# Optimization experiments

Hardware: AMD Instinct MI355X
Metric: run time of the kernel (lower is better)

## Reference

```python
import jax, jax.numpy as jnp
import numpy as np

TREE_DEPTH = 8
N_INTERNAL = 2 ** TREE_DEPTH - 1   # 255
N_LEAVES = 2 ** TREE_DEPTH         # 256
N_CLASSES = 100
N_TREES = 16
BATCH = 8192
D_FEAT = 1024
TEMPERATURE = 1.0


def setup_inputs() -> dict:
    key = jax.random.key(0)
    k1, k2, k3, k4, k5 = jax.random.split(key, 5)
    x = jax.random.normal(k1, (BATCH, D_FEAT), dtype=jnp.float32)
    # scale weights ~1/sqrt(D) so split logits are O(1) (avoids sigmoid saturation)
    split_weights = jax.random.normal(k2, (N_TREES, N_INTERNAL, D_FEAT), dtype=jnp.float32) / np.sqrt(D_FEAT)
    split_bias = jax.random.normal(k3, (N_TREES, N_INTERNAL), dtype=jnp.float32)
    leaf_logits = jax.random.normal(k4, (N_TREES, N_LEAVES, N_CLASSES), dtype=jnp.float32)
    tree_weights = jax.random.normal(k5, (N_TREES,), dtype=jnp.float32)
    return {"x": x, "split_weights": split_weights, "split_bias": split_bias,
            "leaf_logits": leaf_logits, "tree_weights": tree_weights}


def reference(x, split_weights, split_bias, leaf_logits, tree_weights):
    # All internal-node split logits in one contraction: [T, B, N_INTERNAL]
    logits = jnp.einsum('bd,tnd->tbn', x, split_weights) + split_bias[:, None, :]
    split_prob = jax.nn.sigmoid(logits / TEMPERATURE)  # P(go right) per heap node
    T, B = split_prob.shape[0], split_prob.shape[1]
    # Level-order path products. Heap layout: level d occupies nodes [2^d-1, 2^(d+1)-2].
    # Child j of a node splits into (left=2j, right=2j+1) at next level -> interleave.
    mu = jnp.ones((T, B, 1), dtype=x.dtype)
    for d in range(TREE_DEPTH):
        start = 2 ** d - 1
        p = split_prob[:, :, start:start + 2 ** d]          # [T, B, 2^d]
        mu = jnp.stack([mu * (1.0 - p), mu * p], axis=-1)   # left, right
        mu = mu.reshape(T, B, 2 ** (d + 1))
    # mu: [T, B, N_LEAVES] leaf reach probabilities, ordering matches leaf_idx
    leaf_dist = jax.nn.softmax(leaf_logits, axis=-1)        # [T, L, C]
    per_tree = jnp.einsum('tbl,tlc->tbc', mu, leaf_dist)    # [T, B, C]
    w = jax.nn.softmax(tree_weights, axis=0)[:, None, None]
    return (per_tree * w).sum(axis=0)                       # [B, C]
```

## Files before the change

kernel.cpp:

```cpp
#include <hip/hip_runtime.h>
#include <hip/hip_fp16.h>

typedef _Float16 f16;
typedef _Float16 f16x4 __attribute__((ext_vector_type(4)));
typedef _Float16 f16x8 __attribute__((ext_vector_type(8)));
typedef float    f32x4 __attribute__((ext_vector_type(4)));

constexpr int TREES = 16;
constexpr int NNODE = 255;
constexpr int NCLS  = 100;
constexpr int NCPAD = 112;
constexpr int NB    = 8192;
constexpr int DF    = 1024;
constexpr int KTOT  = TREES * 256;

constexpr size_t XH_OFF = 0;
constexpr size_t WH_OFF = XH_OFF + (size_t)NB * DF;
constexpr size_t SD_OFF = WH_OFF + (size_t)TREES * 256 * DF;
constexpr size_t BP_OFF = SD_OFF + (size_t)NCPAD * KTOT;
constexpr size_t PT_OFF_F = (BP_OFF + 8192) / 2;

#define WAIT_VMCNT(n) asm volatile("s_waitcnt vmcnt(" #n ")" ::: "memory")
__device__ __forceinline__ void BAR() {
  asm volatile("" ::: "memory");
  __builtin_amdgcn_s_barrier();
  asm volatile("" ::: "memory");
}

__device__ __forceinline__ void gload_lds16(const f16* g, f16* l) {
  __builtin_amdgcn_global_load_lds(
      (const __attribute__((address_space(1))) void*)g,
      (__attribute__((address_space(3))) void*)l, 16, 0, 0);
}

__global__ void cvt_all_k(const float* __restrict__ x, const float* __restrict__ w,
                          f16* __restrict__ xh, f16* __restrict__ wh) {
  int bid = blockIdx.x;
  if (bid < 4096) {
    int i = bid * 256 + threadIdx.x;
    const float4* s = (const float4*)x + (size_t)i * 2;
    float4 u = s[0], v = s[1];
    f16x8 h = {(f16)u.x, (f16)u.y, (f16)u.z, (f16)u.w,
               (f16)v.x, (f16)v.y, (f16)v.z, (f16)v.w};
    *((f16x8*)xh + i) = h;
  } else {
    int i = (bid - 4096) * 256 + threadIdx.x;
    int flat = i * 8;
    int t = flat >> 18;
    int r = (flat >> 10) & 255;
    int k = flat & 1023;
    f16x8 h;
    if (r < NNODE) {
      const float4* s = (const float4*)(w + ((size_t)(t * NNODE + r) * DF + k));
      float4 u = s[0], v = s[1];
      h = (f16x8){(f16)u.x, (f16)u.y, (f16)u.z, (f16)u.w,
                  (f16)v.x, (f16)v.y, (f16)v.z, (f16)v.w};
    } else {
      h = (f16x8){(f16)0.f, (f16)0.f, (f16)0.f, (f16)0.f,
                  (f16)0.f, (f16)0.f, (f16)0.f, (f16)0.f};
    }
    *((f16x8*)wh + i) = h;
  }
}

__global__ void prep_sdist_k(const float* __restrict__ ll,
                             const float* __restrict__ twin,
                             const float* __restrict__ sb,
                             f16* __restrict__ sdt,
                             float* __restrict__ bp) {
  int wv   = threadIdx.x >> 6;
  int lane = threadIdx.x & 63;
  int id   = blockIdx.x * 4 + wv;
  int t    = id >> 8;
  int node = id & 255;

  float wm = -1e30f;
#pragma unroll
  for (int i = 0; i < 16; ++i) wm = fmaxf(wm, twin[i]);
  float wsum = 0.f;
#pragma unroll
  for (int i = 0; i < 16; ++i) wsum += __expf(twin[i] - wm);
  float wt = __expf(twin[t] - wm) / wsum;

  const float* rowp = ll + (size_t)id * NCLS;
  float v1 = rowp[lane];
  bool has2 = (lane + 64) < NCLS;
  float v2 = has2 ? rowp[lane + 64] : -1e30f;
  float mx = fmaxf(v1, v2);
#pragma unroll
  for (int m = 32; m; m >>= 1) mx = fmaxf(mx, __shfl_xor(mx, m, 64));
  float e1 = __expf(v1 - mx);
  float e2 = has2 ? __expf(v2 - mx) : 0.f;
  float ss = e1 + e2;
#pragma unroll
  for (int m = 32; m; m >>= 1) ss += __shfl_xor(ss, m, 64);
  float inv = wt / ss;

  sdt[(size_t)lane * KTOT + id] = (f16)(e1 * inv);
  if (lane + 64 < NCPAD)
    sdt[(size_t)(lane + 64) * KTOT + id] = has2 ? (f16)(e2 * inv) : (f16)0.f;
  if (lane == 0) bp[id] = (node < NNODE) ? sb[(size_t)t * NNODE + node] : 0.f;
}

__global__ __launch_bounds__(512, 2) void tree_gemm1(
    const f16* __restrict__ xh, const f16* __restrict__ wh,
    const float* __restrict__ biasp, const f16* __restrict__ sdt,
    float* __restrict__ ptree) {
  __shared__ f16 smem[81920];
  char* smb = (char*)smem;

  const int tid  = threadIdx.x;
  const int lane = tid & 63;
  const int wid  = tid >> 6;
  const int l15  = lane & 15;
  const int lq   = lane >> 4;
  const int wrow = (wid >> 2) * 128;
  const int wcol = (wid & 3) * 64;

  int bid  = blockIdx.x;
  int xcd  = bid & 7;
  int idx  = bid >> 3;
  int t    = (xcd & 1) * 8 + (idx & 7);
  int brow = (xcd >> 1) * 8 + (idx >> 3);

  const f16* xsrc = xh + (size_t)brow * 256 * DF;
  const f16* wsrc = wh + (size_t)t * 256 * DF;

  auto stage_half = [&](int kt, int c, int half) {
    f16* Ab = smem + c * 32768;
    f16* Bb = Ab + 16384;
    const f16* xk = xsrc + kt * 64;
    const f16* wk = wsrc + kt * 64;
#pragma unroll
    for (int i = half * 2; i < half * 2 + 2; ++i) {
      int q = i * 512 + tid;
      int r = q >> 3;
      int ci = (q & 7) ^ (r & 7);
      gload_lds16(xk + (size_t)r * DF + ci * 8, Ab + q * 8);
    }
#pragma unroll
    for (int i = half * 2; i < half * 2 + 2; ++i) {
      int q = i * 512 + tid;
      int r = q >> 3;
      int ci = (q & 7) ^ (r & 7);
      gload_lds16(wk + (size_t)r * DF + ci * 8, Bb + q * 8);
    }
  };

  f32x4 acc[8][4];
#pragma unroll
  for (int m = 0; m < 8; ++m)
#pragma unroll
    for (int n = 0; n < 4; ++n) acc[m][n] = (f32x4){0.f, 0.f, 0.f, 0.f};

  stage_half(0, 0, 0);
  stage_half(0, 0, 1);

  for (int kt = 0; kt < 16; ++kt) {
    const int c = kt & 1;
    if (kt < 15) {
      stage_half(kt + 1, c ^ 1, 0);
      WAIT_VMCNT(4);
    } else {
      WAIT_VMCNT(0);
    }
    BAR();

    const char* Ab = smb + c * 65536;
    const char* Bb = Ab + 32768;
#pragma unroll
    for (int s = 0; s < 2; ++s) {
      f16x8 af[8], bf[4];
#pragma unroll
      for (int m = 0; m < 8; ++m) {
        int r = wrow + m * 16 + l15;
        af[m] = *(const f16x8*)(Ab + ((r * 128 + s * 64 + lq * 16) ^ ((r & 7) << 4)));
      }
#pragma unroll
      for (int n = 0; n < 4; ++n) {
        int node = wcol + n * 16 + l15;
        bf[n] = *(const f16x8*)(Bb + ((node * 128 + s * 64 + lq * 16) ^ ((node & 7) << 4)));
      }
      if (s == 0 && kt < 15) stage_half(kt + 1, c ^ 1, 1);
#pragma unroll
      for (int m = 0; m < 8; ++m)
#pragma unroll
        for (int n = 0; n < 4; ++n)
          acc[m][n] = __builtin_amdgcn_mfma_f32_16x16x32_f16(bf[n], af[m], acc[m][n], 0, 0, 0);
    }
    BAR();
  }

  f16x4 ph[8][4];
#pragma unroll
  for (int m = 0; m < 8; ++m) {
#pragma unroll
    for (int n = 0; n < 4; ++n) {
      int col = wcol + n * 16 + lq * 4;
      float4 b4 = *(const float4*)(biasp + t * 256 + col);
#pragma unroll
      for (int reg = 0; reg < 4; ++reg) {
        float bv = (reg == 0) ? b4.x : (reg == 1) ? b4.y : (reg == 2) ? b4.z : b4.w;
        float z = acc[m][n][reg] + bv;
        ph[m][n][reg] = (f16)__builtin_amdgcn_rcpf(1.f + __expf(-z));
      }
    }
  }

  char* Sb = smb;
  char* Ub = smb + 32768;
  char* Pb = smb + 98304;

  auto stage_sdt = [&](int c0, int nrows) {
    int nch = nrows * 32;
    for (int q = tid; q < nch; q += 512) {
      int rr = q >> 5;
      int jj = q & 31;
      gload_lds16(sdt + (size_t)(c0 + rr) * KTOT + t * 256 + ((jj * 8) ^ ((rr & 7) << 3)),
                  smem + q * 8);
    }
  };

  for (int h = 0; h < 2; ++h) {
    if ((wid >> 2) == h) {
#pragma unroll
      for (int m = 0; m < 8; ++m) {
#pragma unroll
        for (int n = 0; n < 4; ++n) {
          int r = m * 16 + l15;
          int colb = (wcol + n * 16 + lq * 4) * 2;
          *(f16x4*)(Pb + ((r * 512 + colb) ^ ((r & 15) << 3))) = ph[m][n];
        }
      }
    }
    __syncthreads();

    {
      int r = tid >> 2;
      int chunk = tid & 3;
      auto PR = [&](int node) -> float {
        return (float)*(const f16*)(Pb + ((r * 512 + node * 2) ^ ((r & 15) << 3)));
      };
      float p0 = PR(0);
      float p1 = PR(1 + (chunk >> 1));
      float pr = ((chunk >> 1) ? p0 : 1.f - p0) * ((chunk & 1) ? p1 : 1.f - p1);
      float p2 = PR(3 + chunk);
      float cur[64];
      {
        float mp = pr * p2;
        cur[1] = mp;
        cur[0] = pr - mp;
      }
#pragma unroll
      for (int d = 3; d <= 7; ++d) {
        int sfan = 1 << (d - 2);
        int nb = (1 << d) - 1 + (chunk << (d - 2));
#pragma unroll
        for (int i = sfan - 1; i >= 0; --i) {
          float p = PR(nb + i);
          float mv = cur[i];
          float mp = mv * p;
          cur[2 * i + 1] = mp;
          cur[2 * i] = mv - mp;
        }
      }
#pragma unroll
      for (int g = 0; g < 8; ++g) {
        f16x8 v;
#pragma unroll
        for (int jj = 0; jj < 8; ++jj) v[jj] = (f16)cur[g * 8 + jj];
        *(f16x8*)(Ub + ((r * 512 + chunk * 128 + g * 16) ^ ((r & 7) << 4))) = v;
      }
    }
    __syncthreads();

    f32x4 acc2[7];
#pragma unroll
    for (int n = 0; n < 7; ++n) acc2[n] = (f32x4){0.f, 0.f, 0.f, 0.f};
    int arow = wid * 16 + l15;

    stage_sdt(0, 64);
    WAIT_VMCNT(0);
    __syncthreads();
#pragma unroll
    for (int n = 0; n < 4; ++n) {
#pragma unroll
      for (int s = 0; s < 8; ++s) {
        f16x8 a = *(const f16x8*)(Ub + ((arow * 512 + s * 64 + lq * 16) ^ ((arow & 7) << 4)));
        int br = n * 16 + l15;
        f16x8 b = *(const f16x8*)(Sb + ((br * 512 + s * 64 + lq * 16) ^ ((br & 7) << 4)));
        acc2[n] = __builtin_amdgcn_mfma_f32_16x16x32_f16(a, b, acc2[n], 0, 0, 0);
      }
    }
    __syncthreads();
    stage_sdt(64, 48);
    WAIT_VMCNT(0);
    __syncthreads();
#pragma unroll
    for (int n = 4; n < 7; ++n) {
#pragma unroll
      for (int s = 0; s < 8; ++s) {
        f16x8 a = *(const f16x8*)(Ub + ((arow * 512 + s * 64 + lq * 16) ^ ((arow & 7) << 4)));
        int br = (n - 4) * 16 + l15;
        f16x8 b = *(const f16x8*)(Sb + ((br * 512 + s * 64 + lq * 16) ^ ((br & 7) << 4)));
        acc2[n] = __builtin_amdgcn_mfma_f32_16x16x32_f16(a, b, acc2[n], 0, 0, 0);
      }
    }

    float* pt = ptree + ((size_t)t * NB + brow * 256 + h * 128) * NCLS;
#pragma unroll
    for (int n = 0; n < 7; ++n) {
      int col = n * 16 + l15;
      if (col < NCLS) {
#pragma unroll
        for (int reg = 0; reg < 4; ++reg) {
          int r = wid * 16 + lq * 4 + reg;
          pt[(size_t)r * NCLS + col] = acc2[n][reg];
        }
      }
    }
    if (h == 0) __syncthreads();
  }
}

__global__ void reduce_k(const float* __restrict__ pt, float* __restrict__ out) {
  int i = blockIdx.x * 256 + threadIdx.x;
  constexpr size_t STRIDE4 = (size_t)NB * NCLS / 4;
  const float4* p = (const float4*)pt + i;
  float4 s = p[0];
#pragma unroll
  for (int t = 1; t < TREES; ++t) {
    float4 v = p[t * STRIDE4];
    s.x += v.x; s.y += v.y; s.z += v.z; s.w += v.w;
  }
  ((float4*)out)[i] = s;
}

extern "C" void kernel_launch(void* const* d_in, const int* in_sizes, int n_in,
                              void* d_out, int out_size, void* d_ws, size_t ws_size,
                              hipStream_t stream) {
  const float* x  = (const float*)d_in[0];
  const float* sw = (const float*)d_in[1];
  const float* sb = (const float*)d_in[2];
  const float* ll = (const float*)d_in[3];
  const float* tw = (const float*)d_in[4];
  float* out = (float*)d_out;

  f16* ws  = (f16*)d_ws;
  f16* xh  = ws + XH_OFF;
  f16* wh  = ws + WH_OFF;
  f16* sdt = ws + SD_OFF;
  float* biasp = (float*)(ws + BP_OFF);
  float* ptree = (float*)d_ws + PT_OFF_F;

  cvt_all_k<<<6144, 256, 0, stream>>>(x, sw, xh, wh);
  prep_sdist_k<<<1024, 256, 0, stream>>>(ll, tw, sb, sdt, biasp);
  tree_gemm1<<<512, 512, 0, stream>>>(xh, wh, biasp, sdt, ptree);
  reduce_k<<<(NB * NCLS / 4) / 256, 256, 0, stream>>>(ptree, out);
}
```

Baseline: 224.8 us.

## Triple-buffer GEMM K-loop, merge prep kernels, prefetch leaf table, vectorize path products

Merges the two preprocessing kernels into one launch. The main GEMM loop moves from a double-buffered 64-wide K step to a triple-buffered 32-wide K step with split loads, explicit lgkmcnt waits, sched barriers and setprio around the MFMA groups. The first leaf-distribution tile is now staged early so its load overlaps the sigmoid and path-product work. The path-product LDS reads are also vectorised with a new swizzle. This adds more barriers per K step and relies on fragile waitcnt counting in exchange for better overlap of loads with compute.

```diff
diff --git a/kernel.cpp b/kernel.cpp
--- a/kernel.cpp
+++ b/kernel.cpp
@@ -21,6 +21,7 @@
 constexpr size_t PT_OFF_F = (BP_OFF + 8192) / 2;
 
 #define WAIT_VMCNT(n) asm volatile("s_waitcnt vmcnt(" #n ")" ::: "memory")
+#define WAIT_LGKM0()  asm volatile("s_waitcnt lgkmcnt(0)" ::: "memory")
 __device__ __forceinline__ void BAR() {
   asm volatile("" ::: "memory");
   __builtin_amdgcn_s_barrier();
@@ -33,8 +34,11 @@
       (__attribute__((address_space(3))) void*)l, 16, 0, 0);
 }
 
-__global__ void cvt_all_k(const float* __restrict__ x, const float* __restrict__ w,
-                          f16* __restrict__ xh, f16* __restrict__ wh) {
+__global__ void prep_all_k(const float* __restrict__ x, const float* __restrict__ w,
+                           const float* __restrict__ ll, const float* __restrict__ twin,
+                           const float* __restrict__ sb,
+                           f16* __restrict__ xh, f16* __restrict__ wh,
+                           f16* __restrict__ sdt, float* __restrict__ bp) {
   int bid = blockIdx.x;
   if (bid < 4096) {
     int i = bid * 256 + threadIdx.x;
@@ -43,7 +47,7 @@
     f16x8 h = {(f16)u.x, (f16)u.y, (f16)u.z, (f16)u.w,
                (f16)v.x, (f16)v.y, (f16)v.z, (f16)v.w};
     *((f16x8*)xh + i) = h;
-  } else {
+  } else if (bid < 6144) {
     int i = (bid - 4096) * 256 + threadIdx.x;
     int flat = i * 8;
     int t = flat >> 18;
@@ -60,46 +64,40 @@
                   (f16)0.f, (f16)0.f, (f16)0.f, (f16)0.f};
     }
     *((f16x8*)wh + i) = h;
+  } else {
+    int wv   = threadIdx.x >> 6;
+    int lane = threadIdx.x & 63;
+    int id   = (bid - 6144) * 4 + wv;
+    int t    = id >> 8;
+    int node = id & 255;
+
+    float wm = -1e30f;
+#pragma unroll
+    for (int i = 0; i < 16; ++i) wm = fmaxf(wm, twin[i]);
+    float wsum = 0.f;
+#pragma unroll
+    for (int i = 0; i < 16; ++i) wsum += __expf(twin[i] - wm);
+    float wt = __expf(twin[t] - wm) / wsum;
+
+    const float* rowp = ll + (size_t)id * NCLS;
+    float v1 = rowp[lane];
+    bool has2 = (lane + 64) < NCLS;
+    float v2 = has2 ? rowp[lane + 64] : -1e30f;
+    float mx = fmaxf(v1, v2);
+#pragma unroll
+    for (int m = 32; m; m >>= 1) mx = fmaxf(mx, __shfl_xor(mx, m, 64));
+    float e1 = __expf(v1 - mx);
+    float e2 = has2 ? __expf(v2 - mx) : 0.f;
+    float ss = e1 + e2;
+#pragma unroll
+    for (int m = 32; m; m >>= 1) ss += __shfl_xor(ss, m, 64);
+    float inv = wt / ss;
+
+    sdt[(size_t)lane * KTOT + id] = (f16)(e1 * inv);
+    if (lane + 64 < NCPAD)
+      sdt[(size_t)(lane + 64) * KTOT + id] = has2 ? (f16)(e2 * inv) : (f16)0.f;
+    if (lane == 0) bp[id] = (node < NNODE) ? sb[(size_t)t * NNODE + node] : 0.f;
   }
-}
-
-__global__ void prep_sdist_k(const float* __restrict__ ll,
-                             const float* __restrict__ twin,
-                             const float* __restrict__ sb,
-                             f16* __restrict__ sdt,
-                             float* __restrict__ bp) {
-  int wv   = threadIdx.x >> 6;
-  int lane = threadIdx.x & 63;
-  int id   = blockIdx.x * 4 + wv;
-  int t    = id >> 8;
-  int node = id & 255;
-
-  float wm = -1e30f;
-#pragma unroll
-  for (int i = 0; i < 16; ++i) wm = fmaxf(wm, twin[i]);
-  float wsum = 0.f;
-#pragma unroll
-  for (int i = 0; i < 16; ++i) wsum += __expf(twin[i] - wm);
-  float wt = __expf(twin[t] - wm) / wsum;
-
-  const float* rowp = ll + (size_t)id * NCLS;
-  float v1 = rowp[lane];
-  bool has2 = (lane + 64) < NCLS;
-  float v2 = has2 ? rowp[lane + 64] : -1e30f;
-  float mx = fmaxf(v1, v2);
-#pragma unroll
-  for (int m = 32; m; m >>= 1) mx = fmaxf(mx, __shfl_xor(mx, m, 64));
-  float e1 = __expf(v1 - mx);
-  float e2 = has2 ? __expf(v2 - mx) : 0.f;
-  float ss = e1 + e2;
-#pragma unroll
-  for (int m = 32; m; m >>= 1) ss += __shfl_xor(ss, m, 64);
-  float inv = wt / ss;
-
-  sdt[(size_t)lane * KTOT + id] = (f16)(e1 * inv);
-  if (lane + 64 < NCPAD)
-    sdt[(size_t)(lane + 64) * KTOT + id] = has2 ? (f16)(e2 * inv) : (f16)0.f;
-  if (lane == 0) bp[id] = (node < NNODE) ? sb[(size_t)t * NNODE + node] : 0.f;
 }
 
 __global__ __launch_bounds__(512, 2) void tree_gemm1(
@@ -126,24 +124,15 @@
   const f16* xsrc = xh + (size_t)brow * 256 * DF;
   const f16* wsrc = wh + (size_t)t * 256 * DF;
 
-  auto stage_half = [&](int kt, int c, int half) {
-    f16* Ab = smem + c * 32768;
-    f16* Bb = Ab + 16384;
-    const f16* xk = xsrc + kt * 64;
-    const f16* wk = wsrc + kt * 64;
-#pragma unroll
-    for (int i = half * 2; i < half * 2 + 2; ++i) {
-      int q = i * 512 + tid;
-      int r = q >> 3;
-      int ci = (q & 7) ^ (r & 7);
-      gload_lds16(xk + (size_t)r * DF + ci * 8, Ab + q * 8);
-    }
-#pragma unroll
-    for (int i = half * 2; i < half * 2 + 2; ++i) {
-      int q = i * 512 + tid;
-      int r = q >> 3;
-      int ci = (q & 7) ^ (r & 7);
-      gload_lds16(wk + (size_t)r * DF + ci * 8, Bb + q * 8);
+  auto stage2 = [&](int kt, int b, int pair) {
+    f16* base = smem + b * 16384 + pair * 8192;
+    const f16* src = (pair == 0 ? xsrc : wsrc) + kt * 32;
+#pragma unroll
+    for (int ch = 0; ch < 2; ++ch) {
+      int u = ch * 512 + tid;
+      int r = u >> 2;
+      int ci = (u & 3) ^ (r & 3);
+      gload_lds16(src + (size_t)r * DF + ci * 8, base + u * 8);
     }
   };
 
@@ -153,58 +142,60 @@
 #pragma unroll
     for (int n = 0; n < 4; ++n) acc[m][n] = (f32x4){0.f, 0.f, 0.f, 0.f};
 
-  stage_half(0, 0, 0);
-  stage_half(0, 0, 1);
-
-  for (int kt = 0; kt < 16; ++kt) {
-    const int c = kt & 1;
-    if (kt < 15) {
-      stage_half(kt + 1, c ^ 1, 0);
-      WAIT_VMCNT(4);
-    } else {
-      WAIT_VMCNT(0);
-    }
+  stage2(0, 0, 0); stage2(0, 0, 1);
+  stage2(1, 1, 0); stage2(1, 1, 1);
+  WAIT_VMCNT(4);
+  BAR();
+
+  for (int kt = 0; kt < 32; ++kt) {
+    const char* Ab = smb + (kt % 3) * 32768;
+    const char* Bb = Ab + 16384;
+    const int nb3 = (kt + 2) % 3;
+    f16x8 af[4], bf[4], ag[4];
+
+#pragma unroll
+    for (int m = 0; m < 4; ++m) {
+      int r = wrow + m * 16 + l15;
+      af[m] = *(const f16x8*)(Ab + ((r * 64 + lq * 16) ^ ((r & 3) << 4)));
+    }
+#pragma unroll
+    for (int n = 0; n < 4; ++n) {
+      int r = wcol + n * 16 + l15;
+      bf[n] = *(const f16x8*)(Bb + ((r * 64 + lq * 16) ^ ((r & 3) << 4)));
+    }
+    if (kt < 30) stage2(kt + 2, nb3, 0);
     BAR();
-
-    const char* Ab = smb + c * 65536;
-    const char* Bb = Ab + 32768;
-#pragma unroll
-    for (int s = 0; s < 2; ++s) {
-      f16x8 af[8], bf[4];
-#pragma unroll
-      for (int m = 0; m < 8; ++m) {
-        int r = wrow + m * 16 + l15;
-        af[m] = *(const f16x8*)(Ab + ((r * 128 + s * 64 + lq * 16) ^ ((r & 7) << 4)));
-      }
-#pragma unroll
-      for (int n = 0; n < 4; ++n) {
-        int node = wcol + n * 16 + l15;
-        bf[n] = *(const f16x8*)(Bb + ((node * 128 + s * 64 + lq * 16) ^ ((node & 7) << 4)));
-      }
-      if (s == 0 && kt < 15) stage_half(kt + 1, c ^ 1, 1);
-#pragma unroll
-      for (int m = 0; m < 8; ++m)
-#pragma unroll
-        for (int n = 0; n < 4; ++n)
-          acc[m][n] = __builtin_amdgcn_mfma_f32_16x16x32_f16(bf[n], af[m], acc[m][n], 0, 0, 0);
-    }
+    WAIT_LGKM0();
+    __builtin_amdgcn_sched_barrier(0);
+    __builtin_amdgcn_s_setprio(1);
+#pragma unroll
+    for (int m = 0; m < 4; ++m)
+#pragma unroll
+      for (int n = 0; n < 4; ++n)
+        acc[m][n] = __builtin_amdgcn_mfma_f32_16x16x32_f16(bf[n], af[m], acc[m][n], 0, 0, 0);
+    __builtin_amdgcn_s_setprio(0);
+    __builtin_amdgcn_sched_barrier(0);
+
+#pragma unroll
+    for (int m = 0; m < 4; ++m) {
+      int r = wrow + 64 + m * 16 + l15;
+      ag[m] = *(const f16x8*)(Ab + ((r * 64 + lq * 16) ^ ((r & 3) << 4)));
+    }
+    if (kt < 30) stage2(kt + 2, nb3, 1);
     BAR();
-  }
-
-  f16x4 ph[8][4];
-#pragma unroll
-  for (int m = 0; m < 8; ++m) {
-#pragma unroll
-    for (int n = 0; n < 4; ++n) {
-      int col = wcol + n * 16 + lq * 4;
-      float4 b4 = *(const float4*)(biasp + t * 256 + col);
-#pragma unroll
-      for (int reg = 0; reg < 4; ++reg) {
-        float bv = (reg == 0) ? b4.x : (reg == 1) ? b4.y : (reg == 2) ? b4.z : b4.w;
-        float z = acc[m][n][reg] + bv;
-        ph[m][n][reg] = (f16)__builtin_amdgcn_rcpf(1.f + __expf(-z));
-      }
-    }
+    WAIT_LGKM0();
+    __builtin_amdgcn_sched_barrier(0);
+    __builtin_amdgcn_s_setprio(1);
+#pragma unroll
+    for (int m = 0; m < 4; ++m)
+#pragma unroll
+      for (int n = 0; n < 4; ++n)
+        acc[m + 4][n] = __builtin_amdgcn_mfma_f32_16x16x32_f16(bf[n], ag[m], acc[m + 4][n], 0, 0, 0);
+    __builtin_amdgcn_s_setprio(0);
+    __builtin_amdgcn_sched_barrier(0);
+
+    if (kt < 30)       { WAIT_VMCNT(4); BAR(); }
+    else if (kt == 30) { WAIT_VMCNT(0); BAR(); }
   }
 
   char* Sb = smb;
@@ -220,6 +211,23 @@
                   smem + q * 8);
     }
   };
+  stage_sdt(0, 64);
+
+  f16x4 ph[8][4];
+#pragma unroll
+  for (int m = 0; m < 8; ++m) {
+#pragma unroll
+    for (int n = 0; n < 4; ++n) {
+      int col = wcol + n * 16 + lq * 4;
+      float4 b4 = *(const float4*)(biasp + t * 256 + col);
+#pragma unroll
+      for (int reg = 0; reg < 4; ++reg) {
+        float bv = (reg == 0) ? b4.x : (reg == 1) ? b4.y : (reg == 2) ? b4.z : b4.w;
+        float z = acc[m][n][reg] + bv;
+        ph[m][n][reg] = (f16)__builtin_amdgcn_rcpf(1.f + __expf(-z));
+      }
+    }
+  }
 
   for (int h = 0; h < 2; ++h) {
     if ((wid >> 2) == h) {
@@ -228,8 +236,8 @@
 #pragma unroll
         for (int n = 0; n < 4; ++n) {
           int r = m * 16 + l15;
-          int colb = (wcol + n * 16 + lq * 4) * 2;
-          *(f16x4*)(Pb + ((r * 512 + colb) ^ ((r & 15) << 3))) = ph[m][n];
+          int nodeb = (wcol + n * 16 + lq * 4) * 2;
+          *(f16x4*)(Pb + ((r * 512 + nodeb) ^ ((r & 7) << 4))) = ph[m][n];
         }
       }
     }
@@ -237,31 +245,83 @@
 
     {
       int r = tid >> 2;
-      int chunk = tid & 3;
-      auto PR = [&](int node) -> float {
-        return (float)*(const f16*)(Pb + ((r * 512 + node * 2) ^ ((r & 15) << 3)));
+      int c = tid & 3;
+      auto PRs = [&](int node) -> float {
+        return (float)*(const f16*)(Pb + ((r * 512 + node * 2) ^ ((r & 7) << 4)));
       };
-      float p0 = PR(0);
-      float p1 = PR(1 + (chunk >> 1));
-      float pr = ((chunk >> 1) ? p0 : 1.f - p0) * ((chunk & 1) ? p1 : 1.f - p1);
-      float p2 = PR(3 + chunk);
+      auto V8 = [&](int node) -> f16x8 {
+        return *(const f16x8*)(Pb + ((r * 512 + node * 2) ^ ((r & 7) << 4)));
+      };
+      float p0 = PRs(0);
+      float p1 = PRs(1 + (c >> 1));
+      float pr = ((c >> 1) ? p0 : 1.f - p0) * ((c & 1) ? p1 : 1.f - p1);
+      float p2 = PRs(3 + c);
       float cur[64];
       {
         float mp = pr * p2;
-        cur[1] = mp;
-        cur[0] = pr - mp;
-      }
-#pragma unroll
-      for (int d = 3; d <= 7; ++d) {
-        int sfan = 1 << (d - 2);
-        int nb = (1 << d) - 1 + (chunk << (d - 2));
-#pragma unroll
-        for (int i = sfan - 1; i >= 0; --i) {
-          float p = PR(nb + i);
-          float mv = cur[i];
-          float mp = mv * p;
-          cur[2 * i + 1] = mp;
-          cur[2 * i] = mv - mp;
+        cur[1] = mp; cur[0] = pr - mp;
+      }
+      {
+        float q0 = PRs(7 + 2 * c), q1 = PRs(8 + 2 * c);
+        float m1 = cur[1], mp1 = m1 * q1;
+        cur[3] = mp1; cur[2] = m1 - mp1;
+        float m0 = cur[0], mp0 = m0 * q0;
+        cur[1] = mp0; cur[0] = m0 - mp0;
+      }
+      {
+        float q[4];
+        q[0] = PRs(15 + 4 * c);
+        f16x4 v = *(const f16x4*)(Pb + ((r * 512 + (16 + 4 * c) * 2) ^ ((r & 7) << 4)));
+        q[1] = (float)v[0]; q[2] = (float)v[1]; q[3] = (float)v[2];
+#pragma unroll
+        for (int i = 3; i >= 0; --i) {
+          float mv = cur[i], mp = mv * q[i];
+          cur[2 * i + 1] = mp; cur[2 * i] = mv - mp;
+        }
+      }
+      {
+        float q[8];
+        q[0] = PRs(31 + 8 * c);
+        f16x8 v = V8(32 + 8 * c);
+#pragma unroll
+        for (int j = 0; j < 7; ++j) q[j + 1] = (float)v[j];
+#pragma unroll
+        for (int i = 7; i >= 0; --i) {
+          float mv = cur[i], mp = mv * q[i];
+          cur[2 * i + 1] = mp; cur[2 * i] = mv - mp;
+        }
+      }
+      {
+        float q[16];
+        q[0] = PRs(63 + 16 * c);
+        f16x8 v0 = V8(64 + 16 * c), v1 = V8(72 + 16 * c);
+#pragma unroll
+        for (int j = 0; j < 8; ++j) q[j + 1] = (float)v0[j];
+#pragma unroll
+        for (int j = 0; j < 7; ++j) q[j + 9] = (float)v1[j];
+#pragma unroll
+        for (int i = 15; i >= 0; --i) {
+          float mv = cur[i], mp = mv * q[i];
+          cur[2 * i + 1] = mp; cur[2 * i] = mv - mp;
+        }
+      }
+      {
+        float q[32];
+        q[0] = PRs(127 + 32 * c);
+        f16x8 v0 = V8(128 + 32 * c), v1 = V8(136 + 32 * c);
+        f16x8 v2 = V8(144 + 32 * c), v3 = V8(152 + 32 * c);
+#pragma unroll
+        for (int j = 0; j < 8; ++j) q[j + 1]  = (float)v0[j];
+#pragma unroll
+        for (int j = 0; j < 8; ++j) q[j + 9]  = (float)v1[j];
+#pragma unroll
+        for (int j = 0; j < 8; ++j) q[j + 17] = (float)v2[j];
+#pragma unroll
+        for (int j = 0; j < 7; ++j) q[j + 25] = (float)v3[j];
+#pragma unroll
+        for (int i = 31; i >= 0; --i) {
+          float mv = cur[i], mp = mv * q[i];
+          cur[2 * i + 1] = mp; cur[2 * i] = mv - mp;
         }
       }
 #pragma unroll
@@ -269,9 +329,10 @@
         f16x8 v;
 #pragma unroll
         for (int jj = 0; jj < 8; ++jj) v[jj] = (f16)cur[g * 8 + jj];
-        *(f16x8*)(Ub + ((r * 512 + chunk * 128 + g * 16) ^ ((r & 7) << 4))) = v;
-      }
-    }
+        *(f16x8*)(Ub + ((r * 512 + c * 128 + g * 16) ^ ((r & 7) << 4))) = v;
+      }
+    }
+    WAIT_VMCNT(0);
     __syncthreads();
 
     f32x4 acc2[7];
@@ -279,9 +340,6 @@
     for (int n = 0; n < 7; ++n) acc2[n] = (f32x4){0.f, 0.f, 0.f, 0.f};
     int arow = wid * 16 + l15;
 
-    stage_sdt(0, 64);
-    WAIT_VMCNT(0);
-    __syncthreads();
 #pragma unroll
     for (int n = 0; n < 4; ++n) {
 #pragma unroll
@@ -319,7 +377,10 @@
         }
       }
     }
-    if (h == 0) __syncthreads();
+    if (h == 0) {
+      __syncthreads();
+      stage_sdt(0, 64);
+    }
   }
 }
 
@@ -353,8 +414,7 @@
   float* biasp = (float*)(ws + BP_OFF);
   float* ptree = (float*)d_ws + PT_OFF_F;
 
-  cvt_all_k<<<6144, 256, 0, stream>>>(x, sw, xh, wh);
-  prep_sdist_k<<<1024, 256, 0, stream>>>(ll, tw, sb, sdt, biasp);
+  prep_all_k<<<7168, 256, 0, stream>>>(x, sw, ll, tw, sb, xh, wh, sdt, biasp);
   tree_gemm1<<<512, 512, 0, stream>>>(xh, wh, biasp, sdt, ptree);
   reduce_k<<<(NB * NCLS / 4) / 256, 256, 0, stream>>>(ptree, out);
 }
```

New measurement: 205.9 us. 8.4% less time.
